# Optimization experiments

Hardware: AMD Instinct MI355X
Metric: run time of the kernel (lower is better)

The kernel has to match this reference:

```python
import jax, jax.numpy as jnp
import numpy as np

REG_COEF = 25.0


def _reflect(points, planes):
    # points: [B,P,3], planes: [B,4] -> reflected points [B,P,3]
    normals = planes[:, 0:3] / jnp.linalg.norm(planes[:, 0:3], axis=1, keepdims=True)
    offsets = planes[:, 3]
    # signed distance of each point to the plane: [B,P]
    dist = jnp.einsum('bd,bpd->bp', normals, points) + offsets[:, None]
    return points - 2.0 * dist[..., None] * normals[:, None, :]


def _chamfer(x, y):
    # x,y: [B,P,3]; pytorch3d chamfer_distance default:
    # mean over points, mean over batch, sum of both directions (squared dists)
    x2 = jnp.sum(x * x, axis=-1)  # [B,P]
    y2 = jnp.sum(y * y, axis=-1)  # [B,P]
    # pairwise squared distances [B,P,P]
    d = x2[:, :, None] + y2[:, None, :] - 2.0 * jnp.einsum('bpd,bqd->bpq', x, y)
    d = jnp.maximum(d, 0.0)
    cham_x = jnp.mean(jnp.min(d, axis=2))  # x -> nearest in y
    cham_y = jnp.mean(jnp.min(d, axis=1))  # y -> nearest in x
    return cham_x + cham_y


def _reg_loss(planes):
    # planes: [B,H,4]
    normals = planes[:, :, :3]
    normals = normals / jnp.linalg.norm(normals, axis=2, keepdims=True)
    H = normals.shape[1]
    a = jnp.einsum('bhd,bgd->bhg', normals, normals) - jnp.eye(H, dtype=normals.dtype)
    # Frobenius norm per batch -> [B]
    return jnp.sqrt(jnp.sum(a * a, axis=(1, 2)))


def setup_inputs() -> dict:
    key = jax.random.key(0)
    k1, k2 = jax.random.split(key)
    B, H, P = 8, 3, 4096
    return {
        'predicted_planes': jax.random.normal(k1, (B, H, 4), dtype=jnp.float32),
        'sample_points': jax.random.normal(k2, (B, P, 3), dtype=jnp.float32),
        'voxel_grids': jnp.zeros((B, 32, 32, 32), dtype=jnp.float32),
        'cp_grids': jnp.zeros((B, 32, 32, 32), dtype=jnp.float32),
    }


def reference(predicted_planes, sample_points, voxel_grids, cp_grids):
    n_heads = predicted_planes.shape[1]
    reg = jnp.sum(_reg_loss(predicted_planes))
    refl = jnp.asarray(0.0, dtype=sample_points.dtype)
    for h in range(n_heads):  # small fixed head count (3)
        reflected = _reflect(sample_points, predicted_planes[:, h, :])
        refl = refl + _chamfer(sample_points, reflected)
    return refl + REG_COEF * reg
```

## Files before the change

### kernel.cpp

```cpp
#include <hip/hip_runtime.h>
#include <math.h>

#define NB 8
#define NH 3
#define NBH 24
#define NP 4096
#define BLK 256
#define RPB 64
#define ROWBLKS (NP / RPB)

typedef _Float16 half4 __attribute__((ext_vector_type(4)));
typedef _Float16 half8 __attribute__((ext_vector_type(8)));
typedef float floatx16 __attribute__((ext_vector_type(16)));

#define MIN3(r, a, b) asm("v_min3_f32 %0, %0, %1, %2" : "+v"(r) : "v"(a), "v"(b))

#define MFMA16(d, a, bb, c) \
    asm("v_mfma_f32_32x32x16_f16 %0, %1, %2, %3" : "=&v"(d) : "v"(a), "v"(bb), "v"(c))

__global__ void __launch_bounds__(256) prep_kernel(const float* __restrict__ pts,
                                                   const float* __restrict__ planes,
                                                   _Float16* __restrict__ qg,
                                                   float* __restrict__ out) {
    const int tid = threadIdx.x;
    const int bh  = blockIdx.x >> 4;
    const int b   = bh / NH;

    const float* pl = planes + bh * 4;
    float n0 = pl[0], n1 = pl[1], n2 = pl[2], off = pl[3];
    float inv = 1.0f / sqrtf(n0 * n0 + n1 * n1 + n2 * n2);
    n0 *= inv; n1 *= inv; n2 *= inv;

    const float* bp = pts + (size_t)b * NP * 3;
    const int i = (blockIdx.x & 15) * 256 + tid;
    {
        float y0 = bp[i * 3 + 0], y1 = bp[i * 3 + 1], y2 = bp[i * 3 + 2];
        float t = 2.0f * (n0 * y0 + n1 * y1 + n2 * y2 + off);
        y0 -= t * n0; y1 -= t * n1; y2 -= t * n2;
        float csq = y0 * y0 + y1 * y1 + y2 * y2;
        half4 q = { (_Float16)(-2.0f * y0), (_Float16)(-2.0f * y1),
                    (_Float16)(-2.0f * y2), (_Float16)csq };
        *(half4*)(qg + ((size_t)bh * NP + i) * 4) = q;
    }

    if (blockIdx.x == 0 && tid >= 192) {
        const int l = tid - 192;
        float r = 0.0f;
        if (l < NB) {
            float n[NH][3];
            for (int hh = 0; hh < NH; ++hh) {
                const float* p2 = planes + (l * NH + hh) * 4;
                float a0 = p2[0], a1 = p2[1], a2 = p2[2];
                float iv = 1.0f / sqrtf(a0 * a0 + a1 * a1 + a2 * a2);
                n[hh][0] = a0 * iv; n[hh][1] = a1 * iv; n[hh][2] = a2 * iv;
            }
            float fro = 0.0f;
            for (int i2 = 0; i2 < NH; ++i2)
                for (int j = 0; j < NH; ++j) {
                    float d = n[i2][0] * n[j][0] + n[i2][1] * n[j][1] + n[i2][2] * n[j][2]
                              - (i2 == j ? 1.0f : 0.0f);
                    fro += d * d;
                }
            r = 25.0f * sqrtf(fro);
        }
        for (int o = 32; o; o >>= 1) r += __shfl_down(r, o);
        if (l == 0) out[0] = r;
    }
}

__global__ void __launch_bounds__(BLK, 4) chamfer_mfma(const float* __restrict__ pts,
                                                       const _Float16* __restrict__ qg,
                                                       float* __restrict__ out) {
    __shared__ float rowmin[2][RPB];

    const int tid  = threadIdx.x;
    const int lane = tid & 63;
    const int wave = tid >> 6;
    const int bh   = blockIdx.y;
    const int b    = bh / NH;
    const int rw   = wave & 1;
    const int cw   = wave >> 1;
    const int h    = lane >> 5;

    const float* bp = pts + (size_t)b * NP * 3;

    const int rlocal = rw * 32 + (lane & 31);
    const int row = blockIdx.x * RPB + rlocal;
    float a0 = bp[row * 3 + 0], a1 = bp[row * 3 + 1], a2 = bp[row * 3 + 2];
    float rsq = a0 * a0 + a1 * a1 + a2 * a2;
    half8 Aev = {0, 0, 0, 0, 0, 0, 0, 0};
    half8 Aod = {0, 0, 0, 0, 0, 0, 0, 0};
    if (lane < 32) {
        Aev[0] = (_Float16)a0; Aev[1] = (_Float16)a1;
        Aev[2] = (_Float16)a2; Aev[3] = (_Float16)1.0f;
        Aod[4] = (_Float16)a0; Aod[5] = (_Float16)a1;
        Aod[6] = (_Float16)a2; Aod[7] = (_Float16)1.0f;
    }

    floatx16 crsq;
    #pragma unroll
    for (int j = 0; j < 16; ++j)
        crsq[j] = __shfl(rsq, (j & 3) + 8 * (j >> 2) + 4 * h);

    float rm[16];
    #pragma unroll
    for (int j = 0; j < 16; ++j) rm[j] = 1e30f;

    const _Float16* bcol = qg + (size_t)bh * NP * 4 + (lane & 31) * 8;
    const int U0 = cw * 32;
    #define LD(u) (*(const half8*)(bcol + (size_t)(u) * 256))

    half8 c0 = LD(U0), c1 = LD(U0 + 1), c2 = LD(U0 + 2), c3 = LD(U0 + 3);
    floatx16 dA0, dA1;
    MFMA16(dA0, Aev, c0, crsq);  MFMA16(dA1, Aod, c0, crsq);

    #pragma unroll 1
    for (int u = U0; u < U0 + 28; u += 4) {
        c0 = LD(u + 4);
        #pragma unroll
        for (int j = 0; j < 16; ++j) MIN3(rm[j], dA0[j], dA1[j]);
        MFMA16(dA0, Aev, c1, crsq);  MFMA16(dA1, Aod, c1, crsq);
        c1 = LD(u + 5);
        #pragma unroll
        for (int j = 0; j < 16; ++j) MIN3(rm[j], dA0[j], dA1[j]);
        MFMA16(dA0, Aev, c2, crsq);  MFMA16(dA1, Aod, c2, crsq);
        c2 = LD(u + 6);
        #pragma unroll
        for (int j = 0; j < 16; ++j) MIN3(rm[j], dA0[j], dA1[j]);
        MFMA16(dA0, Aev, c3, crsq);  MFMA16(dA1, Aod, c3, crsq);
        c3 = LD(u + 7);
        #pragma unroll
        for (int j = 0; j < 16; ++j) MIN3(rm[j], dA0[j], dA1[j]);
        MFMA16(dA0, Aev, c0, crsq);  MFMA16(dA1, Aod, c0, crsq);
    }
    {
        #pragma unroll
        for (int j = 0; j < 16; ++j) MIN3(rm[j], dA0[j], dA1[j]);
        MFMA16(dA0, Aev, c1, crsq);  MFMA16(dA1, Aod, c1, crsq);
        #pragma unroll
        for (int j = 0; j < 16; ++j) MIN3(rm[j], dA0[j], dA1[j]);
        MFMA16(dA0, Aev, c2, crsq);  MFMA16(dA1, Aod, c2, crsq);
        #pragma unroll
        for (int j = 0; j < 16; ++j) MIN3(rm[j], dA0[j], dA1[j]);
        MFMA16(dA0, Aev, c3, crsq);  MFMA16(dA1, Aod, c3, crsq);
        #pragma unroll
        for (int j = 0; j < 16; ++j) MIN3(rm[j], dA0[j], dA1[j]);
    }
    #undef LD

    #pragma unroll
    for (int j = 0; j < 16; ++j) {
        float v = rm[j];
        v = fminf(v, __shfl_xor(v, 1));
        v = fminf(v, __shfl_xor(v, 2));
        v = fminf(v, __shfl_xor(v, 4));
        v = fminf(v, __shfl_xor(v, 8));
        v = fminf(v, __shfl_xor(v, 16));
        rm[j] = v;
    }

    if ((lane & 31) == 0) {
        #pragma unroll
        for (int j = 0; j < 16; ++j)
            rowmin[cw][rw * 32 + (j & 3) + 8 * (j >> 2) + 4 * h] = rm[j];
    }
    __syncthreads();

    if (tid < RPB) {
        float v = fmaxf(fminf(rowmin[0][tid], rowmin[1][tid]), 0.0f);
        #pragma unroll
        for (int o = 32; o; o >>= 1) v += __shfl_down(v, o);
        if (tid == 0) atomicAdd(out, v * (2.0f / (float)(NB * NP)));
    }
}

extern "C" void kernel_launch(void* const* d_in, const int* in_sizes, int n_in,
                              void* d_out, int out_size, void* d_ws, size_t ws_size,
                              hipStream_t stream) {
    const float* planes = (const float*)d_in[0];
    const float* pts    = (const float*)d_in[1];
    float* out          = (float*)d_out;
    _Float16* qg        = (_Float16*)d_ws;

    prep_kernel<<<384, 256, 0, stream>>>(pts, planes, qg, out);

    dim3 grid(ROWBLKS, NBH);
    chamfer_mfma<<<grid, BLK, 0, stream>>>(pts, qg, out);
}
```

Measured before the change: 86.73 us.

## Halve rows per block, zero MFMA accumulator, and double-buffer MFMA results

Each block now covers 32 rows, and its four waves split the columns among themselves instead of using a 2x2 row/column wave layout. This doubles the number of blocks and halves the per-wave column loop. The MFMA no longer takes the shuffled per-row squared norm as its accumulator. It starts from zero and adds the row norm after the min reduction, which removes 16 shuffles per thread. Two independent MFMA result pairs alternate so each min3 pass can overlap the next MFMA's latency, at the cost of more accumulator registers and more atomics.

```diff
diff --git a/kernel.cpp b/kernel.cpp
--- a/kernel.cpp
+++ b/kernel.cpp
@@ -6,7 +6,7 @@
 #define NBH 24
 #define NP 4096
 #define BLK 256
-#define RPB 64
+#define RPB 32
 #define ROWBLKS (NP / RPB)
 
 typedef _Float16 half4 __attribute__((ext_vector_type(4)));
@@ -15,8 +15,8 @@
 
 #define MIN3(r, a, b) asm("v_min3_f32 %0, %0, %1, %2" : "+v"(r) : "v"(a), "v"(b))
 
-#define MFMA16(d, a, bb, c) \
-    asm("v_mfma_f32_32x32x16_f16 %0, %1, %2, %3" : "=&v"(d) : "v"(a), "v"(bb), "v"(c))
+#define MFMA16Z(d, a, bb) \
+    asm("v_mfma_f32_32x32x16_f16 %0, %1, %2, 0" : "=&v"(d) : "v"(a), "v"(bb))
 
 __global__ void __launch_bounds__(256) prep_kernel(const float* __restrict__ pts,
                                                    const float* __restrict__ planes,
@@ -71,23 +71,20 @@
 __global__ void __launch_bounds__(BLK, 4) chamfer_mfma(const float* __restrict__ pts,
                                                        const _Float16* __restrict__ qg,
                                                        float* __restrict__ out) {
-    __shared__ float rowmin[2][RPB];
+    __shared__ float rowmin[4][RPB];
 
     const int tid  = threadIdx.x;
     const int lane = tid & 63;
     const int wave = tid >> 6;
     const int bh   = blockIdx.y;
     const int b    = bh / NH;
-    const int rw   = wave & 1;
-    const int cw   = wave >> 1;
     const int h    = lane >> 5;
 
     const float* bp = pts + (size_t)b * NP * 3;
 
-    const int rlocal = rw * 32 + (lane & 31);
-    const int row = blockIdx.x * RPB + rlocal;
+    const int row = blockIdx.x * RPB + (lane & 31);
     float a0 = bp[row * 3 + 0], a1 = bp[row * 3 + 1], a2 = bp[row * 3 + 2];
-    float rsq = a0 * a0 + a1 * a1 + a2 * a2;
+    float rsqv = a0 * a0 + a1 * a1 + a2 * a2;
     half8 Aev = {0, 0, 0, 0, 0, 0, 0, 0};
     half8 Aod = {0, 0, 0, 0, 0, 0, 0, 0};
     if (lane < 32) {
@@ -97,54 +94,49 @@
         Aod[6] = (_Float16)a2; Aod[7] = (_Float16)1.0f;
     }
 
-    floatx16 crsq;
-    #pragma unroll
-    for (int j = 0; j < 16; ++j)
-        crsq[j] = __shfl(rsq, (j & 3) + 8 * (j >> 2) + 4 * h);
-
     float rm[16];
     #pragma unroll
     for (int j = 0; j < 16; ++j) rm[j] = 1e30f;
 
     const _Float16* bcol = qg + (size_t)bh * NP * 4 + (lane & 31) * 8;
-    const int U0 = cw * 32;
+    const int U0 = wave * 16;
     #define LD(u) (*(const half8*)(bcol + (size_t)(u) * 256))
 
     half8 c0 = LD(U0), c1 = LD(U0 + 1), c2 = LD(U0 + 2), c3 = LD(U0 + 3);
-    floatx16 dA0, dA1;
-    MFMA16(dA0, Aev, c0, crsq);  MFMA16(dA1, Aod, c0, crsq);
+    floatx16 dA0, dA1, dB0, dB1;
+    MFMA16Z(dA0, Aev, c0);  MFMA16Z(dA1, Aod, c0);
+    MFMA16Z(dB0, Aev, c1);  MFMA16Z(dB1, Aod, c1);
 
     #pragma unroll 1
-    for (int u = U0; u < U0 + 28; u += 4) {
+    for (int u = U0; u < U0 + 12; u += 4) {
         c0 = LD(u + 4);
         #pragma unroll
         for (int j = 0; j < 16; ++j) MIN3(rm[j], dA0[j], dA1[j]);
-        MFMA16(dA0, Aev, c1, crsq);  MFMA16(dA1, Aod, c1, crsq);
+        MFMA16Z(dA0, Aev, c2);  MFMA16Z(dA1, Aod, c2);
         c1 = LD(u + 5);
         #pragma unroll
-        for (int j = 0; j < 16; ++j) MIN3(rm[j], dA0[j], dA1[j]);
-        MFMA16(dA0, Aev, c2, crsq);  MFMA16(dA1, Aod, c2, crsq);
+        for (int j = 0; j < 16; ++j) MIN3(rm[j], dB0[j], dB1[j]);
+        MFMA16Z(dB0, Aev, c3);  MFMA16Z(dB1, Aod, c3);
         c2 = LD(u + 6);
         #pragma unroll
         for (int j = 0; j < 16; ++j) MIN3(rm[j], dA0[j], dA1[j]);
-        MFMA16(dA0, Aev, c3, crsq);  MFMA16(dA1, Aod, c3, crsq);
+        MFMA16Z(dA0, Aev, c0);  MFMA16Z(dA1, Aod, c0);
         c3 = LD(u + 7);
         #pragma unroll
-        for (int j = 0; j < 16; ++j) MIN3(rm[j], dA0[j], dA1[j]);
-        MFMA16(dA0, Aev, c0, crsq);  MFMA16(dA1, Aod, c0, crsq);
+        for (int j = 0; j < 16; ++j) MIN3(rm[j], dB0[j], dB1[j]);
+        MFMA16Z(dB0, Aev, c1);  MFMA16Z(dB1, Aod, c1);
     }
     {
         #pragma unroll
         for (int j = 0; j < 16; ++j) MIN3(rm[j], dA0[j], dA1[j]);
-        MFMA16(dA0, Aev, c1, crsq);  MFMA16(dA1, Aod, c1, crsq);
+        MFMA16Z(dA0, Aev, c2);  MFMA16Z(dA1, Aod, c2);
+        #pragma unroll
+        for (int j = 0; j < 16; ++j) MIN3(rm[j], dB0[j], dB1[j]);
+        MFMA16Z(dB0, Aev, c3);  MFMA16Z(dB1, Aod, c3);
         #pragma unroll
         for (int j = 0; j < 16; ++j) MIN3(rm[j], dA0[j], dA1[j]);
-        MFMA16(dA0, Aev, c2, crsq);  MFMA16(dA1, Aod, c2, crsq);
         #pragma unroll
-        for (int j = 0; j < 16; ++j) MIN3(rm[j], dA0[j], dA1[j]);
-        MFMA16(dA0, Aev, c3, crsq);  MFMA16(dA1, Aod, c3, crsq);
-        #pragma unroll
-        for (int j = 0; j < 16; ++j) MIN3(rm[j], dA0[j], dA1[j]);
+        for (int j = 0; j < 16; ++j) MIN3(rm[j], dB0[j], dB1[j]);
     }
     #undef LD
 
@@ -162,14 +154,16 @@
     if ((lane & 31) == 0) {
         #pragma unroll
         for (int j = 0; j < 16; ++j)
-            rowmin[cw][rw * 32 + (j & 3) + 8 * (j >> 2) + 4 * h] = rm[j];
+            rowmin[wave][(j & 3) + 8 * (j >> 2) + 4 * h] = rm[j];
     }
     __syncthreads();
 
     if (tid < RPB) {
-        float v = fmaxf(fminf(rowmin[0][tid], rowmin[1][tid]), 0.0f);
+        float m = fminf(fminf(rowmin[0][tid], rowmin[1][tid]),
+                        fminf(rowmin[2][tid], rowmin[3][tid]));
+        float v = fmaxf(m + rsqv, 0.0f);
         #pragma unroll
-        for (int o = 32; o; o >>= 1) v += __shfl_down(v, o);
+        for (int o = 16; o; o >>= 1) v += __shfl_down(v, o, 32);
         if (tid == 0) atomicAdd(out, v * (2.0f / (float)(NB * NP)));
     }
 }
```

Result: slower. 105.3 us (+21.4%).
